# Optimization experiments

Measured on AMD Instinct MI355X. Metric: run time of the kernel, lower is better.

## Reference

```python
import jax, jax.numpy as jnp
from jax import lax
import numpy as np

D_MODEL = 1024
D_INNER = 2048   # expand=2
D_STATE = 16
D_CONV = 4
DT_RANK = 64     # ceil(1024/16)
N_LAYERS = 24
PATCH = 16
H0 = W0 = 24     # 384 // 16
BATCH = 2
IMG = 384


def setup_inputs() -> dict:
    key = jax.random.key(0)
    ks = jax.random.split(key, 12)
    def rn(k, shape, scale=0.02):
        return jax.random.normal(k, shape, jnp.float32) * scale
    A_init = jnp.broadcast_to(jnp.arange(1, D_STATE + 1, dtype=jnp.float32),
                              (N_LAYERS, D_INNER, D_STATE))
    return {
        "x": jax.random.normal(ks[0], (BATCH, 3, IMG, IMG), jnp.float32),
        "patch_w": rn(ks[1], (D_MODEL, 3, PATCH, PATCH)),
        "patch_b": jnp.zeros((D_MODEL,), jnp.float32),
        "cls_token": rn(ks[2], (1, 1, D_MODEL)),
        "pos_embed": rn(ks[3], (1, 1 + H0 * W0, D_MODEL)),
        "ln_w": jnp.ones((N_LAYERS, D_MODEL), jnp.float32),
        "ln_b": jnp.zeros((N_LAYERS, D_MODEL), jnp.float32),
        "in_proj_w": rn(ks[4], (N_LAYERS, 2 * D_INNER, D_MODEL)),
        "conv_w": rn(ks[5], (N_LAYERS, D_INNER, D_CONV), 0.1),
        "conv_b": jnp.zeros((N_LAYERS, D_INNER), jnp.float32),
        "x_proj_w": rn(ks[6], (N_LAYERS, DT_RANK + 2 * D_STATE, D_INNER)),
        "dt_proj_w": rn(ks[7], (N_LAYERS, D_INNER, DT_RANK), 0.1),
        "dt_proj_b": rn(ks[8], (N_LAYERS, D_INNER), 0.5),
        "A_log": jnp.log(A_init),
        "D_skip": jnp.ones((N_LAYERS, D_INNER), jnp.float32),
        "out_proj_w": rn(ks[9], (N_LAYERS, D_MODEL, D_INNER)),
    }


def _layernorm(x, w, b):
    m = x.mean(-1, keepdims=True)
    xc = x - m
    v = (xc * xc).mean(-1, keepdims=True)
    return xc * lax.rsqrt(v + 1e-5) * w + b


def _mamba_block(tok, p):
    # tok: [B, L, D]
    lw, lb, ipw, cw, cb, xpw, dpw, dpb, alog, dsk, opw = p
    h = _layernorm(tok, lw, lb)
    xz = jnp.einsum('bld,ed->ble', h, ipw)          # [B, L, 2*d_inner]
    xc, z = jnp.split(xz, 2, axis=-1)
    # causal depthwise conv1d over sequence, kernel D_CONV
    u = lax.conv_general_dilated(
        xc.transpose(0, 2, 1), cw[:, None, :], (1,), [(D_CONV - 1, 0)],
        dimension_numbers=('NCH', 'OIH', 'NCH'), feature_group_count=D_INNER)
    u = jax.nn.silu(u + cb[None, :, None]).transpose(0, 2, 1)  # [B, L, d_inner]
    dbl = jnp.einsum('ble,fe->blf', u, xpw)         # [B, L, dt_rank + 2*d_state]
    dt = jax.nn.softplus(jnp.einsum('blr,dr->bld', dbl[..., :DT_RANK], dpw) + dpb)
    Bm = dbl[..., DT_RANK:DT_RANK + D_STATE]        # [B, L, d_state]
    Cm = dbl[..., DT_RANK + D_STATE:]               # [B, L, d_state]
    A = -jnp.exp(alog)                              # [d_inner, d_state]

    def step(hst, inp):
        dt_t, B_t, C_t, u_t = inp                   # [B,d_inner],[B,ds],[B,ds],[B,d_inner]
        hst = jnp.exp(dt_t[..., None] * A) * hst + (dt_t * u_t)[..., None] * B_t[:, None, :]
        y_t = jnp.einsum('bds,bs->bd', hst, C_t)
        return hst, y_t

    h0 = jnp.zeros((tok.shape[0], D_INNER, D_STATE), tok.dtype)
    _, ys = lax.scan(step, h0, (dt.transpose(1, 0, 2), Bm.transpose(1, 0, 2),
                                Cm.transpose(1, 0, 2), u.transpose(1, 0, 2)))
    y = ys.transpose(1, 0, 2) + dsk * u
    y = y * jax.nn.silu(z)
    return tok + jnp.einsum('ble,de->bld', y, opw)


def reference(x, patch_w, patch_b, cls_token, pos_embed, ln_w, ln_b, in_proj_w,
              conv_w, conv_b, x_proj_w, dt_proj_w, dt_proj_b, A_log, D_skip,
              out_proj_w):
    # patch embed: conv stride=kernel=16
    feat = lax.conv_general_dilated(x, patch_w, (PATCH, PATCH), 'VALID',
                                    dimension_numbers=('NCHW', 'OIHW', 'NCHW'))
    feat = feat + patch_b[None, :, None, None]
    B, Dm, H, W = feat.shape
    tokens = feat.reshape(B, Dm, H * W).transpose(0, 2, 1)
    tokens = jnp.concatenate([jnp.broadcast_to(cls_token, (B, 1, Dm)), tokens], 1)
    # bilinear (half-pixel, align_corners=False) pos-embed interpolation
    pp = pos_embed[:, 1:, :].reshape(1, H0, W0, Dm)
    pp = jax.image.resize(pp, (1, H, W, Dm), method='bilinear').reshape(1, H * W, Dm)
    tokens = tokens + jnp.concatenate([pos_embed[:, :1, :], pp], 1)
    params = (ln_w, ln_b, in_proj_w, conv_w, conv_b, x_proj_w, dt_proj_w,
              dt_proj_b, A_log, D_skip, out_proj_w)
    blk = jax.checkpoint(_mamba_block)
    tokens, _ = lax.scan(lambda t, p: (blk(t, p), None), tokens, params)
    return tokens
```

## Files before the change

kernel.cpp:

```cpp
#include <hip/hip_runtime.h>
#include <hip/hip_bf16.h>
#include <math.h>

#define BATCH 2
#define LSEQ 577
#define DM 1024
#define DI 2048
#define DSTATE 16
#define DTR 64
#define NLAYERS 24
#define NP 576
#define MROWS 1154
#define NC 32
#define LC 19

typedef __attribute__((ext_vector_type(8))) short short8v;
typedef __attribute__((ext_vector_type(4))) float f32x4;

__device__ __forceinline__ ushort f2bf(float f) {
  unsigned int b = __float_as_uint(f);
  return (ushort)((b + 0x7FFFu + ((b >> 16) & 1u)) >> 16);
}
__device__ __forceinline__ float bf2f(ushort u) {
  return __uint_as_float(((unsigned int)u) << 16);
}
__device__ __forceinline__ void gload16(const void* g, void* l) {
  __builtin_amdgcn_global_load_lds(
      (const __attribute__((address_space(1))) unsigned int*)g,
      (__attribute__((address_space(3))) unsigned int*)l, 16, 0, 0);
}
__device__ __forceinline__ void cvt16(const float* g, char* ldsrow, int bb, int bswz) {
  float4 v0 = *(const float4*)(g);
  float4 v1 = *(const float4*)(g + 4);
  float4 v2 = *(const float4*)(g + 8);
  float4 v3 = *(const float4*)(g + 12);
  short8v c0 = {(short)f2bf(v0.x), (short)f2bf(v0.y), (short)f2bf(v0.z), (short)f2bf(v0.w),
                (short)f2bf(v1.x), (short)f2bf(v1.y), (short)f2bf(v1.z), (short)f2bf(v1.w)};
  short8v c1 = {(short)f2bf(v2.x), (short)f2bf(v2.y), (short)f2bf(v2.z), (short)f2bf(v2.w),
                (short)f2bf(v3.x), (short)f2bf(v3.y), (short)f2bf(v3.z), (short)f2bf(v3.w)};
  *(short8v*)(ldsrow + (bb ^ bswz)) = c0;
  *(short8v*)(ldsrow + ((bb + 16) ^ bswz)) = c1;
}

__global__ void f2bf_k(const float* __restrict__ in, ushort* __restrict__ out, int n) {
  for (int i = (blockIdx.x * 256 + threadIdx.x) * 4; i < n; i += gridDim.x * 1024) {
    float4 v = *(const float4*)(in + i);
    ushort4 o;
    o.x = f2bf(v.x); o.y = f2bf(v.y); o.z = f2bf(v.z); o.w = f2bf(v.w);
    *(ushort4*)(out + i) = o;
  }
}

template<int AF32, int MODE>
__global__ __launch_bounds__(256) void gemm64(
    const void* __restrict__ Ap_, int lda,
    const ushort* __restrict__ Bw, int ldb,
    float* __restrict__ C, int ldc,
    int M, int N, int K,
    const float* __restrict__ bias, const float* __restrict__ pos,
    ushort* __restrict__ o16a, ushort* __restrict__ o16b)
{
  __shared__ char lds[24576];
  int tid = threadIdx.x;
  int lane = tid & 63, w = tid >> 6;
  int bm = blockIdx.y * 64, bn = blockIdx.x * 128;

  int srow = tid >> 3;
  int scol = ((tid & 7) ^ (srow & 7)) << 3;

  const ushort* gb0 = Bw + (size_t)(bn + srow) * ldb + scol;
  const ushort* gb1 = Bw + (size_t)(bn + 32 + srow) * ldb + scol;
  const ushort* gb2 = Bw + (size_t)(bn + 64 + srow) * ldb + scol;
  const ushort* gb3 = Bw + (size_t)(bn + 96 + srow) * ldb + scol;
  char* lb0 = lds + 8192 + (w << 10);
  char* lb1 = lds + 12288 + (w << 10);
  char* lb2 = lds + 16384 + (w << 10);
  char* lb3 = lds + 20480 + (w << 10);

  const ushort* ga0 = nullptr; const ushort* ga1 = nullptr;
  char* la0 = lds + (w << 10);
  char* la1 = lds + 4096 + (w << 10);
  const float* gAf = nullptr; char* ldsArow = nullptr; int bb = 0, bswz = 0;
  if (!AF32) {
    const ushort* Abf = (const ushort*)Ap_;
    int ra0 = bm + srow;      if (ra0 > M - 1) ra0 = M - 1;
    int ra1 = bm + 32 + srow; if (ra1 > M - 1) ra1 = M - 1;
    ga0 = Abf + (size_t)ra0 * lda + scol;
    ga1 = Abf + (size_t)ra1 * lda + scol;
  } else {
    int brow = tid >> 2;
    int be0 = (tid & 3) << 4;
    bb = be0 << 1; bswz = (brow & 7) << 4;
    int raf = bm + brow; if (raf > M - 1) raf = M - 1;
    gAf = (const float*)Ap_ + (size_t)raf * lda + be0;
    ldsArow = lds + brow * 128;
  }

  int wr = w >> 1, wc = w & 1;
  int fr = lane & 15;
  int fsw = (fr & 7) << 4;
  int fk = (lane >> 4) << 4;

  f32x4 acc[2][4];
  #pragma unroll
  for (int m = 0; m < 2; ++m)
    #pragma unroll
    for (int n = 0; n < 4; ++n) acc[m][n] = (f32x4){0.f, 0.f, 0.f, 0.f};

  for (int k0 = 0; k0 < K; k0 += 64) {
    if (!AF32) {
      gload16(ga0 + k0, la0);
      gload16(ga1 + k0, la1);
    } else {
      cvt16(gAf + k0, ldsArow, bb, bswz);
    }
    gload16(gb0 + k0, lb0);
    gload16(gb1 + k0, lb1);
    gload16(gb2 + k0, lb2);
    gload16(gb3 + k0, lb3);
    __syncthreads();
    #pragma unroll
    for (int ks = 0; ks < 2; ++ks) {
      int cb = (ks * 64 + fk) ^ fsw;
      short8v af[2], bf[4];
      #pragma unroll
      for (int m = 0; m < 2; ++m)
        af[m] = *(const short8v*)(lds + (wr * 32 + m * 16 + fr) * 128 + cb);
      #pragma unroll
      for (int n = 0; n < 4; ++n)
        bf[n] = *(const short8v*)(lds + 8192 + (wc * 64 + n * 16 + fr) * 128 + cb);
      #pragma unroll
      for (int m = 0; m < 2; ++m)
        #pragma unroll
        for (int n = 0; n < 4; ++n)
          acc[m][n] = __builtin_amdgcn_mfma_f32_16x16x32_bf16(af[m], bf[n], acc[m][n], 0, 0, 0);
    }
    __syncthreads();
  }

  #pragma unroll
  for (int m = 0; m < 2; ++m) {
    int rb = bm + wr * 32 + m * 16 + ((lane >> 4) << 2);
    #pragma unroll
    for (int j = 0; j < 4; ++j) {
      int r = rb + j;
      if (r >= M) break;
      #pragma unroll
      for (int n2 = 0; n2 < 4; ++n2) {
        int n = bn + wc * 64 + n2 * 16 + fr;
        float v = acc[m][n2][j];
        if (MODE == 1) {
          C[(size_t)r * ldc + n] += v;
        } else if (MODE == 3) {
          int b = r / NP, p = r % NP;
          C[((size_t)(b * LSEQ + 1 + p)) * ldc + n] = v + bias[n] + pos[(size_t)(1 + p) * ldc + n];
        } else if (MODE == 4) {
          if (n < DI) o16a[(size_t)r * DI + n] = f2bf(v);
          else        o16b[(size_t)r * DI + n - DI] = f2bf(v);
        } else {
          float t = v + bias[n];
          o16a[(size_t)r * N + n] = f2bf((t > 20.f) ? t : log1pf(__expf(t)));
        }
      }
    }
  }
}

__global__ __launch_bounds__(256) void xproj_k(
    const ushort* __restrict__ A, const ushort* __restrict__ W,
    float* __restrict__ C, int M)
{
  __shared__ char lds[20480];
  int tid = threadIdx.x;
  int lane = tid & 63, w = tid >> 6;
  int bm = blockIdx.y * 64;
  int kbase = blockIdx.x * 256;

  int srow = tid >> 3;
  int scol = ((tid & 7) ^ (srow & 7)) << 3;
  int ra0 = bm + srow;      if (ra0 > M - 1) ra0 = M - 1;
  int ra1 = bm + 32 + srow; if (ra1 > M - 1) ra1 = M - 1;
  const ushort* ga0 = A + (size_t)ra0 * DI + kbase + scol;
  const ushort* ga1 = A + (size_t)ra1 * DI + kbase + scol;
  char* la0 = lds + (w << 10);
  char* la1 = lds + 4096 + (w << 10);
  const ushort* gb0 = W + (size_t)(srow)      * DI + kbase + scol;
  const ushort* gb1 = W + (size_t)(srow + 32) * DI + kbase + scol;
  const ushort* gb2 = W + (size_t)(srow + 64) * DI + kbase + scol;
  char* lb0 = lds + 8192 + (w << 10);
  char* lb1 = lds + 12288 + (w << 10);
  char* lb2 = lds + 16384 + (w << 10);

  int fr = lane & 15;
  int fsw = (fr & 7) << 4;
  int fk = (lane >> 4) << 4;
  int arow = (w * 16 + fr) * 128;

  f32x4 acc[6];
  #pragma unroll
  for (int n = 0; n < 6; ++n) acc[n] = (f32x4){0.f, 0.f, 0.f, 0.f};

  for (int k0 = 0; k0 < 256; k0 += 64) {
    gload16(ga0 + k0, la0);
    gload16(ga1 + k0, la1);
    gload16(gb0 + k0, lb0);
    gload16(gb1 + k0, lb1);
    gload16(gb2 + k0, lb2);
    __syncthreads();
    #pragma unroll
    for (int ks = 0; ks < 2; ++ks) {
      int cb = (ks * 64 + fk) ^ fsw;
      short8v af = *(const short8v*)(lds + arow + cb);
      #pragma unroll
      for (int n = 0; n < 6; ++n) {
        short8v bf = *(const short8v*)(lds + 8192 + (n * 16 + fr) * 128 + cb);
        acc[n] = __builtin_amdgcn_mfma_f32_16x16x32_bf16(af, bf, acc[n], 0, 0, 0);
      }
    }
    __syncthreads();
  }

  int rb = bm + w * 16 + ((lane >> 4) << 2);
  #pragma unroll
  for (int j = 0; j < 4; ++j) {
    int r = rb + j;
    if (r >= M) break;
    #pragma unroll
    for (int n = 0; n < 6; ++n)
      atomicAdd(C + (size_t)r * 96 + n * 16 + fr, acc[n][j]);
  }
}

__global__ void im2col_k(const float* __restrict__ x, ushort* __restrict__ patches) {
  int idx = blockIdx.x * 256 + threadIdx.x;
  if (idx >= BATCH * NP * 768) return;
  int col = idx % 768, row = idx / 768;
  int b = row / NP, p = row % NP;
  int ph = p / 24, pw = p % 24;
  int c = col >> 8, r = col & 255, kh = r >> 4, kw = r & 15;
  patches[idx] = f2bf(x[(((size_t)(b * 3 + c) * 384) + ph * 16 + kh) * 384 + pw * 16 + kw]);
}

__global__ void cls_k(const float* __restrict__ cls, const float* __restrict__ pos,
                      float* __restrict__ out) {
  int n = blockIdx.x * 256 + threadIdx.x;
  if (n >= DM) return;
  float v = cls[n] + pos[n];
  out[n] = v;
  out[(size_t)LSEQ * DM + n] = v;
}

__global__ __launch_bounds__(256) void ln_k(const float* __restrict__ tok,
    const float* __restrict__ w, const float* __restrict__ bsh,
    ushort* __restrict__ h) {
  int row = blockIdx.x;
  const float* xr = tok + (size_t)row * DM;
  int tid = threadIdx.x;
  float v[4];
  #pragma unroll
  for (int i = 0; i < 4; ++i) v[i] = xr[tid + 256 * i];
  float s = v[0] + v[1] + v[2] + v[3];
  float s2 = v[0] * v[0] + v[1] * v[1] + v[2] * v[2] + v[3] * v[3];
  #pragma unroll
  for (int off = 32; off; off >>= 1) { s += __shfl_xor(s, off); s2 += __shfl_xor(s2, off); }
  __shared__ float ps[4], ps2[4];
  if ((tid & 63) == 0) { ps[tid >> 6] = s; ps2[tid >> 6] = s2; }
  __syncthreads();
  s = ps[0] + ps[1] + ps[2] + ps[3];
  s2 = ps2[0] + ps2[1] + ps2[2] + ps2[3];
  float mean = s * (1.f / DM);
  float var = s2 * (1.f / DM) - mean * mean;
  float inv = rsqrtf(var + 1e-5f);
  #pragma unroll
  for (int i = 0; i < 4; ++i) {
    int c = tid + 256 * i;
    h[(size_t)row * DM + c] = f2bf((v[i] - mean) * inv * w[c] + bsh[c]);
  }
}

__global__ void conv_silu_k(const ushort* __restrict__ xc, const float* __restrict__ cw,
                            const float* __restrict__ cb, ushort* __restrict__ ubf,
                            float* __restrict__ dbl0) {
  int idx = blockIdx.x * 256 + threadIdx.x;
  if (idx < MROWS * 96) dbl0[idx] = 0.f;
  if (idx >= MROWS * DI) return;
  int d = idx & (DI - 1);
  int ro = idx >> 11;
  int l = ro % LSEQ;
  float acc = cb[d];
  #pragma unroll
  for (int k = 0; k < 4; ++k) {
    int ll = l - 3 + k;
    if (ll >= 0) acc += bf2f(xc[(size_t)(ro - 3 + k) * DI + d]) * cw[d * 4 + k];
  }
  ubf[idx] = f2bf(acc / (1.f + __expf(-acc)));
}

__global__ __launch_bounds__(256) void scan1_k(
    const ushort* __restrict__ dt, const ushort* __restrict__ ubf,
    const float* __restrict__ dbl, const float* __restrict__ alog,
    ushort* __restrict__ Ap, ushort* __restrict__ He)
{
  int d = blockIdx.x * 256 + threadIdx.x;
  int b = blockIdx.y, c = blockIdx.z;
  int t0 = c * LC, t1 = t0 + LC; if (t1 > LSEQ) t1 = LSEQ;
  float Ad[DSTATE], ap[DSTATE], h[DSTATE];
  #pragma unroll
  for (int s = 0; s < DSTATE; ++s) {
    Ad[s] = -__expf(alog[d * DSTATE + s]); ap[s] = 1.f; h[s] = 0.f;
  }
  for (int t = t0; t < t1; ++t) {
    size_t ro = (size_t)b * LSEQ + t;
    float dtv = bf2f(dt[ro * DI + d]);
    float du = dtv * bf2f(ubf[ro * DI + d]);
    const float* r = dbl + ro * 96;
    #pragma unroll
    for (int s = 0; s < DSTATE; ++s) {
      float e = __expf(dtv * Ad[s]);
      h[s] = e * h[s] + du * r[64 + s];
      ap[s] *= e;
    }
  }
  size_t o = (((size_t)(b * NC + c)) * DI + d) * DSTATE;
  #pragma unroll
  for (int s = 0; s < DSTATE; ++s) { Ap[o + s] = f2bf(ap[s]); He[o + s] = f2bf(h[s]); }
}

__global__ __launch_bounds__(256) void scan2_k(
    ushort* __restrict__ Ap, const ushort* __restrict__ He)
{
  int ds = blockIdx.x * 256 + threadIdx.x;
  int b = blockIdx.y;
  float h = 0.f;
  for (int c = 0; c < NC; ++c) {
    size_t o = ((size_t)(b * NC + c)) * DI * DSTATE + ds;
    float ap = bf2f(Ap[o]), he = bf2f(He[o]);
    Ap[o] = f2bf(h);
    h = ap * h + he;
  }
}

__global__ __launch_bounds__(256) void scan3_k(
    const ushort* __restrict__ dt, const ushort* __restrict__ ubf,
    const float* __restrict__ dbl, const ushort* __restrict__ zbf,
    const float* __restrict__ alog, const float* __restrict__ dsk,
    const ushort* __restrict__ H0, ushort* __restrict__ y)
{
  int d = blockIdx.x * 256 + threadIdx.x;
  int b = blockIdx.y, c = blockIdx.z;
  int t0 = c * LC, t1 = t0 + LC; if (t1 > LSEQ) t1 = LSEQ;
  float Ad[DSTATE], h[DSTATE];
  size_t o = (((size_t)(b * NC + c)) * DI + d) * DSTATE;
  #pragma unroll
  for (int s = 0; s < DSTATE; ++s) {
    Ad[s] = -__expf(alog[d * DSTATE + s]);
    h[s] = bf2f(H0[o + s]);
  }
  float Dv = dsk[d];
  for (int t = t0; t < t1; ++t) {
    size_t ro = (size_t)b * LSEQ + t;
    float dtv = bf2f(dt[ro * DI + d]);
    float uv = bf2f(ubf[ro * DI + d]);
    float du = dtv * uv;
    const float* r = dbl + ro * 96;
    float yv = 0.f;
    #pragma unroll
    for (int s = 0; s < DSTATE; ++s) {
      h[s] = __expf(dtv * Ad[s]) * h[s] + du * r[64 + s];
      yv += h[s] * r[80 + s];
    }
    float z = bf2f(zbf[ro * DI + d]);
    y[ro * DI + d] = f2bf((yv + Dv * uv) * (z / (1.f + __expf(-z))));
  }
}

extern "C" void kernel_launch(void* const* d_in, const int* in_sizes, int n_in,
                              void* d_out, int out_size, void* d_ws, size_t ws_size,
                              hipStream_t stream) {
  const float* x         = (const float*)d_in[0];
  const float* patch_w   = (const float*)d_in[1];
  const float* patch_b   = (const float*)d_in[2];
  const float* cls_token = (const float*)d_in[3];
  const float* pos_embed = (const float*)d_in[4];
  const float* ln_w      = (const float*)d_in[5];
  const float* ln_b      = (const float*)d_in[6];
  const float* in_proj_w = (const float*)d_in[7];
  const float* conv_w    = (const float*)d_in[8];
  const float* conv_b    = (const float*)d_in[9];
  const float* x_proj_w  = (const float*)d_in[10];
  const float* dt_proj_w = (const float*)d_in[11];
  const float* dt_proj_b = (const float*)d_in[12];
  const float* A_log     = (const float*)d_in[13];
  const float* D_skip    = (const float*)d_in[14];
  const float* out_proj_w= (const float*)d_in[15];
  float* tok = (float*)d_out;

  char* base = (char*)d_ws;
  ushort* xc_bf  = (ushort*)(base);
  ushort* z_bf   = (ushort*)(base + 4726784);
  ushort* u_bf   = (ushort*)(base + 9453568);
  float*  dbl    = (float*)(base + 14180352);
  ushort* dt_bf  = (ushort*)(base + 14623488);
  ushort* h_bf   = (ushort*)(base + 19350272);
  ushort* y_bf   = (ushort*)(base + 21713664);
  ushort* Ap     = (ushort*)(base + 26440448);
  ushort* He     = (ushort*)(base + 30634752);
  ushort* wpatch = (ushort*)(base + 34829056);
  ushort* wxp    = (ushort*)(base + 36401920);
  ushort* wdt    = (ushort*)(base + 45839104);
  ushort* wout   = (ushort*)(base + 52130560);
  ushort* win    = (ushort*)(base + 152793856);
  ushort* patches= (ushort*)u_bf;

  f2bf_k<<<4096, 256, 0, stream>>>(patch_w,   wpatch, 1024 * 768);
  f2bf_k<<<4096, 256, 0, stream>>>(x_proj_w,  wxp,    NLAYERS * 96 * DI);
  f2bf_k<<<4096, 256, 0, stream>>>(dt_proj_w, wdt,    NLAYERS * DI * DTR);
  f2bf_k<<<8192, 256, 0, stream>>>(out_proj_w,wout,   NLAYERS * DM * DI);
  f2bf_k<<<8192, 256, 0, stream>>>(in_proj_w, win,    NLAYERS * 2 * DI * DM);

  im2col_k<<<(BATCH * NP * 768 + 255) / 256, 256, 0, stream>>>(x, patches);
  {
    dim3 gp(DM / 128, (BATCH * NP) / 64);
    gemm64<0, 3><<<gp, 256, 0, stream>>>(patches, 768, wpatch, 768, tok, DM,
                                         BATCH * NP, DM, 768, patch_b, pos_embed,
                                         nullptr, nullptr);
  }
  cls_k<<<(DM + 255) / 256, 256, 0, stream>>>(cls_token, pos_embed, tok);

  for (int l = 0; l < NLAYERS; ++l) {
    ln_k<<<MROWS, 256, 0, stream>>>(tok, ln_w + l * DM, ln_b + l * DM, h_bf);

    {
      dim3 g1(2 * DI / 128, (MROWS + 63) / 64);
      gemm64<0, 4><<<g1, 256, 0, stream>>>(h_bf, DM, win + (size_t)l * 2 * DI * DM, DM,
                                           nullptr, 0, MROWS, 2 * DI, DM,
                                           nullptr, nullptr, xc_bf, z_bf);
    }

    conv_silu_k<<<(MROWS * DI + 255) / 256, 256, 0, stream>>>(
        xc_bf, conv_w + (size_t)l * DI * 4, conv_b + (size_t)l * DI, u_bf, dbl);

    {
      dim3 g2(8, (MROWS + 63) / 64);
      xproj_k<<<g2, 256, 0, stream>>>(u_bf, wxp + (size_t)l * 96 * DI, dbl, MROWS);
    }

    {
      dim3 g3(DI / 128, (MROWS + 63) / 64);
      gemm64<1, 5><<<g3, 256, 0, stream>>>(dbl, 96, wdt + (size_t)l * DI * DTR, DTR,
                                           nullptr, 0, MROWS, DI, DTR,
                                           dt_proj_b + (size_t)l * DI, nullptr, dt_bf, nullptr);
    }

    {
      dim3 gs(DI / 256, BATCH, NC);
      scan1_k<<<gs, 256, 0, stream>>>(dt_bf, u_bf, dbl,
                                      A_log + (size_t)l * DI * DSTATE, Ap, He);
      dim3 gs2(DI * DSTATE / 256, BATCH);
      scan2_k<<<gs2, 256, 0, stream>>>(Ap, He);
      scan3_k<<<gs, 256, 0, stream>>>(dt_bf, u_bf, dbl, z_bf,
                                      A_log + (size_t)l * DI * DSTATE, D_skip + (size_t)l * DI,
                                      Ap, y_bf);
    }

    {
      dim3 g4(DM / 128, (MROWS + 63) / 64);
      gemm64<0, 1><<<g4, 256, 0, stream>>>(y_bf, DI, wout + (size_t)l * DM * DI, DI,
                                           tok, DM, MROWS, DM, DI, nullptr, nullptr,
                                           nullptr, nullptr);
    }
  }
}
```

Measured before the change: 3.570 ms.

## Fuse three-pass chunked selective scan into one cooperative kernel with grid syncs

Replaces the three chunked-scan kernels (per-chunk partial scan, cross-chunk carry, final scan with output) with a single cooperative kernel that uses two grid-wide syncs between phases. The dt and u values loaded in phase one are packed into registers and reused in phase three instead of being reloaded from global memory. This removes two launches per layer and some redundant global reads, but adds grid-sync cost, a 512-block cooperative grid that must be fully co-resident, and extra register pressure from the 19-entry packed array.

Measured after the change: 9.342 ms. 2.62x slower.

```diff
diff --git a/kernel.cpp b/kernel.cpp
--- a/kernel.cpp
+++ b/kernel.cpp
@@ -1,5 +1,6 @@
 #include <hip/hip_runtime.h>
 #include <hip/hip_bf16.h>
+#include <hip/hip_cooperative_groups.h>
 #include <math.h>
 
 #define BATCH 2
@@ -13,6 +14,8 @@
 #define MROWS 1154
 #define NC 32
 #define LC 19
+
+namespace cg = cooperative_groups;
 
 typedef __attribute__((ext_vector_type(8))) short short8v;
 typedef __attribute__((ext_vector_type(4))) float f32x4;
@@ -296,81 +299,97 @@
   ubf[idx] = f2bf(acc / (1.f + __expf(-acc)));
 }
 
-__global__ __launch_bounds__(256) void scan1_k(
-    const ushort* __restrict__ dt, const ushort* __restrict__ ubf,
-    const float* __restrict__ dbl, const float* __restrict__ alog,
-    ushort* __restrict__ Ap, ushort* __restrict__ He)
-{
-  int d = blockIdx.x * 256 + threadIdx.x;
-  int b = blockIdx.y, c = blockIdx.z;
-  int t0 = c * LC, t1 = t0 + LC; if (t1 > LSEQ) t1 = LSEQ;
-  float Ad[DSTATE], ap[DSTATE], h[DSTATE];
-  #pragma unroll
-  for (int s = 0; s < DSTATE; ++s) {
-    Ad[s] = -__expf(alog[d * DSTATE + s]); ap[s] = 1.f; h[s] = 0.f;
-  }
-  for (int t = t0; t < t1; ++t) {
-    size_t ro = (size_t)b * LSEQ + t;
-    float dtv = bf2f(dt[ro * DI + d]);
-    float du = dtv * bf2f(ubf[ro * DI + d]);
-    const float* r = dbl + ro * 96;
-    #pragma unroll
-    for (int s = 0; s < DSTATE; ++s) {
-      float e = __expf(dtv * Ad[s]);
-      h[s] = e * h[s] + du * r[64 + s];
-      ap[s] *= e;
-    }
-  }
-  size_t o = (((size_t)(b * NC + c)) * DI + d) * DSTATE;
-  #pragma unroll
-  for (int s = 0; s < DSTATE; ++s) { Ap[o + s] = f2bf(ap[s]); He[o + s] = f2bf(h[s]); }
-}
-
-__global__ __launch_bounds__(256) void scan2_k(
-    ushort* __restrict__ Ap, const ushort* __restrict__ He)
-{
-  int ds = blockIdx.x * 256 + threadIdx.x;
-  int b = blockIdx.y;
-  float h = 0.f;
-  for (int c = 0; c < NC; ++c) {
-    size_t o = ((size_t)(b * NC + c)) * DI * DSTATE + ds;
-    float ap = bf2f(Ap[o]), he = bf2f(He[o]);
-    Ap[o] = f2bf(h);
-    h = ap * h + he;
-  }
-}
-
-__global__ __launch_bounds__(256) void scan3_k(
+__global__ __launch_bounds__(256) void scanf_k(
     const ushort* __restrict__ dt, const ushort* __restrict__ ubf,
     const float* __restrict__ dbl, const ushort* __restrict__ zbf,
     const float* __restrict__ alog, const float* __restrict__ dsk,
-    const ushort* __restrict__ H0, ushort* __restrict__ y)
+    ushort* __restrict__ Ap, ushort* __restrict__ He, ushort* __restrict__ y)
 {
-  int d = blockIdx.x * 256 + threadIdx.x;
+  cg::grid_group grid = cg::this_grid();
+  int tid = threadIdx.x;
+  int d = blockIdx.x * 256 + tid;
   int b = blockIdx.y, c = blockIdx.z;
   int t0 = c * LC, t1 = t0 + LC; if (t1 > LSEQ) t1 = LSEQ;
-  float Ad[DSTATE], h[DSTATE];
+
+  float Ad[DSTATE], ap[DSTATE], h[DSTATE];
+  #pragma unroll
+  for (int s = 0; s < DSTATE; ++s) {
+    Ad[s] = -__expf(alog[d * DSTATE + s]); ap[s] = 1.f; h[s] = 0.f;
+  }
+  unsigned pk[LC];
+  #pragma unroll
+  for (int tt = 0; tt < LC; ++tt) {
+    int t = t0 + tt;
+    if (t < t1) {
+      size_t ro = (size_t)b * LSEQ + t;
+      ushort ds_ = dt[ro * DI + d];
+      ushort us_ = ubf[ro * DI + d];
+      pk[tt] = ((unsigned)us_ << 16) | ds_;
+      float dtv = bf2f(ds_), du = dtv * bf2f(us_);
+      const float* r = dbl + ro * 96;
+      #pragma unroll
+      for (int s = 0; s < DSTATE; ++s) {
+        float e = __expf(dtv * Ad[s]);
+        h[s] = e * h[s] + du * r[64 + s];
+        ap[s] *= e;
+      }
+    } else {
+      pk[tt] = 0;
+    }
+  }
   size_t o = (((size_t)(b * NC + c)) * DI + d) * DSTATE;
   #pragma unroll
-  for (int s = 0; s < DSTATE; ++s) {
-    Ad[s] = -__expf(alog[d * DSTATE + s]);
-    h[s] = bf2f(H0[o + s]);
-  }
+  for (int s = 0; s < DSTATE; ++s) { Ap[o + s] = f2bf(ap[s]); He[o + s] = f2bf(h[s]); }
+
+  __threadfence();
+  grid.sync();
+
+  int bid = blockIdx.x + blockIdx.y * 8 + blockIdx.z * 16;
+  if (bid < 256) {
+    int tg = bid * 256 + tid;
+    int b2 = tg >> 15, ds2 = tg & 32767;
+    float hh = 0.f;
+    #pragma unroll
+    for (int g = 0; g < 4; ++g) {
+      float apg[8], heg[8];
+      #pragma unroll
+      for (int j = 0; j < 8; ++j) {
+        size_t oo = ((size_t)(b2 * NC + g * 8 + j)) * DI * DSTATE + ds2;
+        apg[j] = bf2f(Ap[oo]); heg[j] = bf2f(He[oo]);
+      }
+      #pragma unroll
+      for (int j = 0; j < 8; ++j) {
+        size_t oo = ((size_t)(b2 * NC + g * 8 + j)) * DI * DSTATE + ds2;
+        Ap[oo] = f2bf(hh);
+        hh = apg[j] * hh + heg[j];
+      }
+    }
+  }
+
+  __threadfence();
+  grid.sync();
+
+  #pragma unroll
+  for (int s = 0; s < DSTATE; ++s) h[s] = bf2f(Ap[o + s]);
   float Dv = dsk[d];
-  for (int t = t0; t < t1; ++t) {
-    size_t ro = (size_t)b * LSEQ + t;
-    float dtv = bf2f(dt[ro * DI + d]);
-    float uv = bf2f(ubf[ro * DI + d]);
-    float du = dtv * uv;
-    const float* r = dbl + ro * 96;
-    float yv = 0.f;
-    #pragma unroll
-    for (int s = 0; s < DSTATE; ++s) {
-      h[s] = __expf(dtv * Ad[s]) * h[s] + du * r[64 + s];
-      yv += h[s] * r[80 + s];
-    }
-    float z = bf2f(zbf[ro * DI + d]);
-    y[ro * DI + d] = f2bf((yv + Dv * uv) * (z / (1.f + __expf(-z))));
+  #pragma unroll
+  for (int tt = 0; tt < LC; ++tt) {
+    int t = t0 + tt;
+    if (t < t1) {
+      size_t ro = (size_t)b * LSEQ + t;
+      float dtv = bf2f((ushort)(pk[tt] & 0xFFFFu));
+      float uv  = bf2f((ushort)(pk[tt] >> 16));
+      float du = dtv * uv;
+      const float* r = dbl + ro * 96;
+      float yv = 0.f;
+      #pragma unroll
+      for (int s = 0; s < DSTATE; ++s) {
+        h[s] = __expf(dtv * Ad[s]) * h[s] + du * r[64 + s];
+        yv += h[s] * r[80 + s];
+      }
+      float z = bf2f(zbf[ro * DI + d]);
+      y[ro * DI + d] = f2bf((yv + Dv * uv) * (z / (1.f + __expf(-z))));
+    }
   }
 }
 
@@ -453,14 +472,18 @@
     }
 
     {
-      dim3 gs(DI / 256, BATCH, NC);
-      scan1_k<<<gs, 256, 0, stream>>>(dt_bf, u_bf, dbl,
-                                      A_log + (size_t)l * DI * DSTATE, Ap, He);
-      dim3 gs2(DI * DSTATE / 256, BATCH);
-      scan2_k<<<gs2, 256, 0, stream>>>(Ap, He);
-      scan3_k<<<gs, 256, 0, stream>>>(dt_bf, u_bf, dbl, z_bf,
-                                      A_log + (size_t)l * DI * DSTATE, D_skip + (size_t)l * DI,
-                                      Ap, y_bf);
+      const ushort* dtp = dt_bf;
+      const ushort* up  = u_bf;
+      const float*  dblp = dbl;
+      const ushort* zp  = z_bf;
+      const float*  alp = A_log + (size_t)l * DI * DSTATE;
+      const float*  dsp = D_skip + (size_t)l * DI;
+      ushort* App = Ap; ushort* Hep = He; ushort* yp = y_bf;
+      void* args[] = {(void*)&dtp, (void*)&up, (void*)&dblp, (void*)&zp,
+                      (void*)&alp, (void*)&dsp, (void*)&App, (void*)&Hep, (void*)&yp};
+      dim3 gs(8, 2, 32);
+      hipLaunchCooperativeKernel(reinterpret_cast<void*>(scanf_k), gs, dim3(256),
+                                 args, 0, stream);
     }
 
     {
```

## Double-buffer LDS in bf16 GEMM and batch loads in scan2

Applied to the files above, without the earlier changes.

For bf16-A GEMMs the LDS is doubled and the K loop now prefetches the next tile into the alternate buffer. Explicit vmcnt waits and raw barriers let global-to-LDS loads overlap MFMA compute. The chunk-carry scan kernel now loads 8 chunks at a time before the serial recurrence, to expose memory-level parallelism. The cost is twice the LDS per block (48KB), which may reduce occupancy, and the hand-written vmcnt count depends on how many memory instructions gload16 emits.

Measured after the change: 3.074 ms. -13.9%, faster.

```diff
diff --git a/kernel.cpp b/kernel.cpp
--- a/kernel.cpp
+++ b/kernel.cpp
@@ -60,7 +60,7 @@
     const float* __restrict__ bias, const float* __restrict__ pos,
     ushort* __restrict__ o16a, ushort* __restrict__ o16b)
 {
-  __shared__ char lds[24576];
+  __shared__ char lds[AF32 ? 24576 : 49152];
   int tid = threadIdx.x;
   int lane = tid & 63, w = tid >> 6;
   int bm = blockIdx.y * 64, bn = blockIdx.x * 128;
@@ -72,14 +72,8 @@
   const ushort* gb1 = Bw + (size_t)(bn + 32 + srow) * ldb + scol;
   const ushort* gb2 = Bw + (size_t)(bn + 64 + srow) * ldb + scol;
   const ushort* gb3 = Bw + (size_t)(bn + 96 + srow) * ldb + scol;
-  char* lb0 = lds + 8192 + (w << 10);
-  char* lb1 = lds + 12288 + (w << 10);
-  char* lb2 = lds + 16384 + (w << 10);
-  char* lb3 = lds + 20480 + (w << 10);
 
   const ushort* ga0 = nullptr; const ushort* ga1 = nullptr;
-  char* la0 = lds + (w << 10);
-  char* la1 = lds + 4096 + (w << 10);
   const float* gAf = nullptr; char* ldsArow = nullptr; int bb = 0, bswz = 0;
   if (!AF32) {
     const ushort* Abf = (const ushort*)Ap_;
@@ -107,35 +101,72 @@
     #pragma unroll
     for (int n = 0; n < 4; ++n) acc[m][n] = (f32x4){0.f, 0.f, 0.f, 0.f};
 
-  for (int k0 = 0; k0 < K; k0 += 64) {
-    if (!AF32) {
-      gload16(ga0 + k0, la0);
-      gload16(ga1 + k0, la1);
-    } else {
-      cvt16(gAf + k0, ldsArow, bb, bswz);
-    }
-    gload16(gb0 + k0, lb0);
-    gload16(gb1 + k0, lb1);
-    gload16(gb2 + k0, lb2);
-    gload16(gb3 + k0, lb3);
-    __syncthreads();
-    #pragma unroll
-    for (int ks = 0; ks < 2; ++ks) {
-      int cb = (ks * 64 + fk) ^ fsw;
-      short8v af[2], bf[4];
+  if constexpr (!AF32) {
+    auto stage = [&](int buf, int k0) {
+      char* p = lds + buf * 24576;
+      gload16(ga0 + k0, p + (w << 10));
+      gload16(ga1 + k0, p + 4096 + (w << 10));
+      gload16(gb0 + k0, p + 8192 + (w << 10));
+      gload16(gb1 + k0, p + 12288 + (w << 10));
+      gload16(gb2 + k0, p + 16384 + (w << 10));
+      gload16(gb3 + k0, p + 20480 + (w << 10));
+    };
+    int nk = K >> 6;
+    stage(0, 0);
+    for (int k = 0; k < nk; ++k) {
+      int cur = k & 1;
+      if (k + 1 < nk) {
+        stage(cur ^ 1, (k + 1) << 6);
+        asm volatile("s_waitcnt vmcnt(6)" ::: "memory");
+      } else {
+        asm volatile("s_waitcnt vmcnt(0)" ::: "memory");
+      }
+      __builtin_amdgcn_s_barrier();
+      char* p = lds + cur * 24576;
       #pragma unroll
-      for (int m = 0; m < 2; ++m)
-        af[m] = *(const short8v*)(lds + (wr * 32 + m * 16 + fr) * 128 + cb);
-      #pragma unroll
-      for (int n = 0; n < 4; ++n)
-        bf[n] = *(const short8v*)(lds + 8192 + (wc * 64 + n * 16 + fr) * 128 + cb);
-      #pragma unroll
-      for (int m = 0; m < 2; ++m)
+      for (int ks = 0; ks < 2; ++ks) {
+        int cb = (ks * 64 + fk) ^ fsw;
+        short8v af[2], bf[4];
+        #pragma unroll
+        for (int m = 0; m < 2; ++m)
+          af[m] = *(const short8v*)(p + (wr * 32 + m * 16 + fr) * 128 + cb);
         #pragma unroll
         for (int n = 0; n < 4; ++n)
-          acc[m][n] = __builtin_amdgcn_mfma_f32_16x16x32_bf16(af[m], bf[n], acc[m][n], 0, 0, 0);
-    }
-    __syncthreads();
+          bf[n] = *(const short8v*)(p + 8192 + (wc * 64 + n * 16 + fr) * 128 + cb);
+        #pragma unroll
+        for (int m = 0; m < 2; ++m)
+          #pragma unroll
+          for (int n = 0; n < 4; ++n)
+            acc[m][n] = __builtin_amdgcn_mfma_f32_16x16x32_bf16(af[m], bf[n], acc[m][n], 0, 0, 0);
+      }
+      __builtin_amdgcn_s_barrier();
+    }
+  } else {
+    for (int k0 = 0; k0 < K; k0 += 64) {
+      cvt16(gAf + k0, ldsArow, bb, bswz);
+      gload16(gb0 + k0, lds + 8192 + (w << 10));
+      gload16(gb1 + k0, lds + 12288 + (w << 10));
+      gload16(gb2 + k0, lds + 16384 + (w << 10));
+      gload16(gb3 + k0, lds + 20480 + (w << 10));
+      __syncthreads();
+      #pragma unroll
+      for (int ks = 0; ks < 2; ++ks) {
+        int cb = (ks * 64 + fk) ^ fsw;
+        short8v af[2], bf[4];
+        #pragma unroll
+        for (int m = 0; m < 2; ++m)
+          af[m] = *(const short8v*)(lds + (wr * 32 + m * 16 + fr) * 128 + cb);
+        #pragma unroll
+        for (int n = 0; n < 4; ++n)
+          bf[n] = *(const short8v*)(lds + 8192 + (wc * 64 + n * 16 + fr) * 128 + cb);
+        #pragma unroll
+        for (int m = 0; m < 2; ++m)
+          #pragma unroll
+          for (int n = 0; n < 4; ++n)
+            acc[m][n] = __builtin_amdgcn_mfma_f32_16x16x32_bf16(af[m], bf[n], acc[m][n], 0, 0, 0);
+      }
+      __syncthreads();
+    }
   }
 
   #pragma unroll
@@ -332,11 +363,20 @@
   int ds = blockIdx.x * 256 + threadIdx.x;
   int b = blockIdx.y;
   float h = 0.f;
-  for (int c = 0; c < NC; ++c) {
-    size_t o = ((size_t)(b * NC + c)) * DI * DSTATE + ds;
-    float ap = bf2f(Ap[o]), he = bf2f(He[o]);
-    Ap[o] = f2bf(h);
-    h = ap * h + he;
+  #pragma unroll
+  for (int g = 0; g < NC; g += 8) {
+    float apg[8], heg[8];
+    #pragma unroll
+    for (int j = 0; j < 8; ++j) {
+      size_t oo = ((size_t)(b * NC + g + j)) * DI * DSTATE + ds;
+      apg[j] = bf2f(Ap[oo]); heg[j] = bf2f(He[oo]);
+    }
+    #pragma unroll
+    for (int j = 0; j < 8; ++j) {
+      size_t oo = ((size_t)(b * NC + g + j)) * DI * DSTATE + ds;
+      Ap[oo] = f2bf(h);
+      h = apg[j] * h + heg[j];
+    }
   }
 }
 
```
